# Kernel optimization log

Measured on AMD Instinct MI355X. Metric: run time of the kernel, lower is better.

## Reference

```python
import jax, jax.numpy as jnp
import numpy as np
import math

# Dims chosen per input_specs
B, Q, S, T = 8, 64, 64, 64          # batch, queries, stat (segment) count, tokens per segment
H, DH = 8, 64                        # heads, head dim
NH = H * DH                          # num_hiddens = 512
STAT_K, TOKEN_K = 8, 16
NEG = -1e6


def setup_inputs() -> dict:
    key = jax.random.key(0)
    ks = jax.random.split(key, 11)
    f = lambda k, sh: jax.random.normal(k, sh, dtype=jnp.float32)
    w = lambda k: f(k, (NH, NH)) * 0.05  # Linear weights stored as [in, out]
    return {
        "queries": f(ks[0], (B, Q, NH)),
        "stat_keys": f(ks[1], (B, S, NH)),
        "token_keys": f(ks[2], (B * S, T, NH)),
        "values": f(ks[3], (B * S, T, NH)),
        "stat_valid_lens": jax.random.randint(ks[4], (B,), 1, S + 1, dtype=jnp.int32),
        "Wq_stat": w(ks[5]),
        "Wq_token": w(ks[6]),
        "Wk_stat": w(ks[7]),
        "Wk_token": w(ks[8]),
        "Wv": w(ks[9]),
        "Wo": w(ks[10]),
    }


def reference(queries, stat_keys, token_keys, values, stat_valid_lens,
              Wq_stat, Wq_token, Wk_stat, Wk_token, Wv, Wo):
    scale = 1.0 / math.sqrt(DH)

    def split_heads(x):  # [b, L, H*DH] -> [b, H, L, DH]
        b, L, _ = x.shape
        return x.reshape(b, L, H, DH).transpose(0, 2, 1, 3)

    q_stat = split_heads(queries @ Wq_stat)        # [B,H,Q,DH]
    q_tok = split_heads(queries @ Wq_token)        # [B,H,Q,DH]
    k_stat = split_heads(stat_keys @ Wk_stat)      # [B,H,S,DH]
    # token_keys/values come in as [B*S, T, size]; per-head layout [B,H,S,T,DH]
    k_tok = (token_keys @ Wk_token).reshape(B, S, T, H, DH).transpose(0, 3, 1, 2, 4)
    v = (values @ Wv).reshape(B, S, T, H, DH).transpose(0, 3, 1, 2, 4)

    # --- stat-level scores, valid-length mask, top-k sparsification, softmax ---
    stat_scores = jnp.einsum('bhqd,bhsd->bhqs', q_stat, k_stat) * scale  # [B,H,Q,S]
    valid = jnp.arange(S)[None, None, None, :] < stat_valid_lens[:, None, None, None]
    stat_scores = jnp.where(valid, stat_scores, NEG)
    k1 = min(S - 1, STAT_K)
    _, top_idx = jax.lax.top_k(stat_scores, k1)                           # [B,H,Q,k1]
    keep = jax.nn.one_hot(top_idx, S, dtype=stat_scores.dtype).sum(-2) > 0  # [B,H,Q,S]
    stat_w = jax.nn.softmax(jnp.where(keep, stat_scores, NEG), axis=-1)   # [B,H,Q,S]

    # --- token-level scores. NOTE: the original code computes torch.topk but then
    # overwrites with the LAST k2 positions (token_weights[:, :, -k2:] = ...), so the
    # token top-k result is dead code; we faithfully reproduce the last-k2 masking. ---
    tok_scores = jnp.einsum('bhqd,bhstd->bhsqt', q_tok, k_tok) * scale    # [B,H,S,Q,T]
    k2 = min(T - 1, TOKEN_K)
    last_mask = jnp.arange(T) >= (T - k2)
    tok_w = jax.nn.softmax(jnp.where(last_mask, tok_scores, NEG), axis=-1)
    tok_w = tok_w.transpose(0, 1, 3, 2, 4)                                # [B,H,Q,S,T]

    # --- combine hierarchy and attend over values ---
    comb = stat_w[..., None] * tok_w                                      # [B,H,Q,S,T]
    out = jnp.einsum('bhqst,bhstd->bhqd', comb, v)                        # [B,H,Q,DH]
    out = out.transpose(0, 2, 1, 3).reshape(B, Q, NH)
    return out @ Wo
```

## Files before the change

### kernel.cpp

```cpp
#include <hip/hip_runtime.h>
#include <hip/hip_bf16.h>

#define BB 8
#define QQ 64
#define SS 64
#define TT 64
#define HH 8
#define DH 64
#define NHID 512
#define STAT_K 8
#define TOKEN_K 16

typedef short bf16x8 __attribute__((ext_vector_type(8)));
typedef float f32x4 __attribute__((ext_vector_type(4)));

__device__ inline ushort f2bf_rne(float x) {
    union { float f; unsigned u; } v; v.f = x;
    unsigned r = v.u + 0x7fff + ((v.u >> 16) & 1);
    return (ushort)(r >> 16);
}
__device__ inline float bf2f(ushort h) {
    union { unsigned u; float f; } v; v.u = ((unsigned)h) << 16;
    return v.f;
}

__global__ __launch_bounds__(256) void conv_all(
    const float* w0, const float* w1, const float* w2,
    const float* w3, const float* w4, const float* w5,
    const float* queries, const float* stat_keys,
    ushort* wT, ushort* q_hi, ushort* q_lo, ushort* sk_hi, ushort* sk_lo)
{
    const int z = blockIdx.z;
    if (z < 6) {
        const float* srcs[6] = {w0, w1, w2, w3, w4, w5};
        const float* src = srcs[z];
        ushort* hi = wT + (size_t)z * 524288;
        ushort* lo = hi + 262144;
        __shared__ float t[32][33];
        const int c0 = blockIdx.x * 32, r0 = blockIdx.y * 32;
        const int tx = threadIdx.x & 31, ty = threadIdx.x >> 5;
        #pragma unroll
        for (int i = 0; i < 4; ++i)
            t[ty + 8 * i][tx] = src[(r0 + ty + 8 * i) * 512 + c0 + tx];
        __syncthreads();
        #pragma unroll
        for (int i = 0; i < 4; ++i) {
            float x = t[tx][ty + 8 * i];
            ushort h = f2bf_rne(x);
            int o = (c0 + ty + 8 * i) * 512 + r0 + tx;
            hi[o] = h;
            lo[o] = f2bf_rne(x - bf2f(h));
        }
    } else {
        const float* src = (z == 6) ? queries : stat_keys;
        ushort* hi = (z == 6) ? q_hi : sk_hi;
        ushort* lo = (z == 6) ? q_lo : sk_lo;
        int base = (blockIdx.y * 16 + blockIdx.x) * 1024 + threadIdx.x * 4;
        float4 x = *(const float4*)(src + base);
        ushort4 h, l;
        h.x = f2bf_rne(x.x); l.x = f2bf_rne(x.x - bf2f(h.x));
        h.y = f2bf_rne(x.y); l.y = f2bf_rne(x.y - bf2f(h.y));
        h.z = f2bf_rne(x.z); l.z = f2bf_rne(x.z - bf2f(h.z));
        h.w = f2bf_rne(x.w); l.w = f2bf_rne(x.w - bf2f(h.w));
        *(ushort4*)(hi + base) = h;
        *(ushort4*)(lo + base) = l;
    }
}

__global__ __launch_bounds__(256) void gemm_split3(
    const ushort* __restrict__ q_hi, const ushort* __restrict__ q_lo,
    const ushort* __restrict__ sk_hi, const ushort* __restrict__ sk_lo,
    const ushort* __restrict__ wT,
    float* __restrict__ q_stat, float* __restrict__ k_stat,
    float* __restrict__ q_tokf)
{
    const int z = blockIdx.z;
    const ushort* Ah = (z == 1) ? sk_hi : q_hi;
    const ushort* Al = (z == 1) ? sk_lo : q_lo;
    const ushort* Bh = wT + (size_t)z * 524288;
    const ushort* Bl = Bh + 262144;
    float* C = (z == 0) ? q_stat : (z == 1) ? k_stat : q_tokf;
    const int K = 512, N = 512;

    __shared__ ushort As[2][64][40];
    __shared__ ushort Bs[2][64][40];
    const int tid = threadIdx.x;
    const int row0 = blockIdx.y * 64, col0 = blockIdx.x * 64;
    const int wave = tid >> 6, lane = tid & 63;
    const int wm = wave & 1, wn = wave >> 1;
    const int m16 = lane & 15, quad = lane >> 4;
    const int srow = tid >> 2, schunk = tid & 3;

    f32x4 acc[2][2];
    #pragma unroll
    for (int i = 0; i < 2; ++i)
        #pragma unroll
        for (int j = 0; j < 2; ++j)
            #pragma unroll
            for (int r = 0; r < 4; ++r) acc[i][j][r] = 0.f;

    for (int k0 = 0; k0 < K; k0 += 32) {
        const size_t aoff = (size_t)(row0 + srow) * K + k0 + schunk * 8;
        const size_t boff = (size_t)(col0 + srow) * K + k0 + schunk * 8;
        *(uint4*)&As[0][srow][schunk * 8] = *(const uint4*)(Ah + aoff);
        *(uint4*)&Bs[0][srow][schunk * 8] = *(const uint4*)(Bh + boff);
        *(uint4*)&As[1][srow][schunk * 8] = *(const uint4*)(Al + aoff);
        *(uint4*)&Bs[1][srow][schunk * 8] = *(const uint4*)(Bl + boff);
        __syncthreads();

        bf16x8 af[2], bf[2], afl[2], bfl[2];
        #pragma unroll
        for (int i = 0; i < 2; ++i) {
            af[i]  = *(const bf16x8*)&As[0][wm * 32 + i * 16 + m16][quad * 8];
            bf[i]  = *(const bf16x8*)&Bs[0][wn * 32 + i * 16 + m16][quad * 8];
            afl[i] = *(const bf16x8*)&As[1][wm * 32 + i * 16 + m16][quad * 8];
            bfl[i] = *(const bf16x8*)&Bs[1][wn * 32 + i * 16 + m16][quad * 8];
        }
        #pragma unroll
        for (int i = 0; i < 2; ++i)
            #pragma unroll
            for (int j = 0; j < 2; ++j) {
                acc[i][j] = __builtin_amdgcn_mfma_f32_16x16x32_bf16(af[i], bf[j], acc[i][j], 0, 0, 0);
                acc[i][j] = __builtin_amdgcn_mfma_f32_16x16x32_bf16(af[i], bfl[j], acc[i][j], 0, 0, 0);
                acc[i][j] = __builtin_amdgcn_mfma_f32_16x16x32_bf16(afl[i], bf[j], acc[i][j], 0, 0, 0);
            }
        __syncthreads();
    }

    #pragma unroll
    for (int i = 0; i < 2; ++i)
        #pragma unroll
        for (int j = 0; j < 2; ++j) {
            int r0 = row0 + wm * 32 + i * 16 + quad * 4;
            int c = col0 + wn * 32 + j * 16 + m16;
            #pragma unroll
            for (int reg = 0; reg < 4; ++reg)
                C[(size_t)(r0 + reg) * N + c] = acc[i][j][reg];
        }
}

__global__ __launch_bounds__(256) void gemm_out(
    const ushort* __restrict__ Ah, const ushort* __restrict__ Al,
    const ushort* __restrict__ Bh, const ushort* __restrict__ Bl,
    float* __restrict__ C)
{
    const int K = 512, N = 512;
    __shared__ ushort As[2][64][40];
    __shared__ ushort Bs[2][64][40];
    const int tid = threadIdx.x;
    const int row0 = blockIdx.y * 64, col0 = blockIdx.x * 64;
    const int wave = tid >> 6, lane = tid & 63;
    const int wm = wave & 1, wn = wave >> 1;
    const int m16 = lane & 15, quad = lane >> 4;
    const int srow = tid >> 2, schunk = tid & 3;

    f32x4 acc[2][2];
    #pragma unroll
    for (int i = 0; i < 2; ++i)
        #pragma unroll
        for (int j = 0; j < 2; ++j)
            #pragma unroll
            for (int r = 0; r < 4; ++r) acc[i][j][r] = 0.f;

    for (int k0 = 0; k0 < K; k0 += 32) {
        const size_t aoff = (size_t)(row0 + srow) * K + k0 + schunk * 8;
        const size_t boff = (size_t)(col0 + srow) * K + k0 + schunk * 8;
        *(uint4*)&As[0][srow][schunk * 8] = *(const uint4*)(Ah + aoff);
        *(uint4*)&Bs[0][srow][schunk * 8] = *(const uint4*)(Bh + boff);
        *(uint4*)&As[1][srow][schunk * 8] = *(const uint4*)(Al + aoff);
        *(uint4*)&Bs[1][srow][schunk * 8] = *(const uint4*)(Bl + boff);
        __syncthreads();

        bf16x8 af[2], bf[2], afl[2], bfl[2];
        #pragma unroll
        for (int i = 0; i < 2; ++i) {
            af[i]  = *(const bf16x8*)&As[0][wm * 32 + i * 16 + m16][quad * 8];
            bf[i]  = *(const bf16x8*)&Bs[0][wn * 32 + i * 16 + m16][quad * 8];
            afl[i] = *(const bf16x8*)&As[1][wm * 32 + i * 16 + m16][quad * 8];
            bfl[i] = *(const bf16x8*)&Bs[1][wn * 32 + i * 16 + m16][quad * 8];
        }
        #pragma unroll
        for (int i = 0; i < 2; ++i)
            #pragma unroll
            for (int j = 0; j < 2; ++j) {
                acc[i][j] = __builtin_amdgcn_mfma_f32_16x16x32_bf16(af[i], bf[j], acc[i][j], 0, 0, 0);
                acc[i][j] = __builtin_amdgcn_mfma_f32_16x16x32_bf16(af[i], bfl[j], acc[i][j], 0, 0, 0);
                acc[i][j] = __builtin_amdgcn_mfma_f32_16x16x32_bf16(afl[i], bf[j], acc[i][j], 0, 0, 0);
            }
        __syncthreads();
    }

    #pragma unroll
    for (int i = 0; i < 2; ++i)
        #pragma unroll
        for (int j = 0; j < 2; ++j) {
            int r0 = row0 + wm * 32 + i * 16 + quad * 4;
            int c = col0 + wn * 32 + j * 16 + m16;
            #pragma unroll
            for (int reg = 0; reg < 4; ++reg)
                C[(size_t)(r0 + reg) * N + c] = acc[i][j][reg];
        }
}

__global__ __launch_bounds__(256) void gemm_tok(
    const float* __restrict__ token_keys, const float* __restrict__ values,
    const ushort* __restrict__ wkt_h, const ushort* __restrict__ wv_h,
    ushort* __restrict__ k_tok, ushort* __restrict__ v_proj)
{
    const int z = blockIdx.z;
    const float* A = z ? values : token_keys;
    const ushort* Bh = z ? wv_h : wkt_h;
    ushort* C = z ? v_proj : k_tok;
    const int K = 512, N = 512;

    __shared__ ushort As[64][40];
    __shared__ ushort Bs[256][40];
    const int tid = threadIdx.x;
    const int row0 = blockIdx.y * 64, col0 = blockIdx.x * 256;
    const int wave = tid >> 6, lane = tid & 63;
    const int m16 = lane & 15, quad = lane >> 4;
    const int srow = tid >> 2, schunk = tid & 3;

    const int r = row0 + srow;
    const size_t arow = (size_t)((r >> 4) * 64 + 48 + (r & 15)) * K;

    f32x4 acc[4][4];
    #pragma unroll
    for (int i = 0; i < 4; ++i)
        #pragma unroll
        for (int j = 0; j < 4; ++j)
            #pragma unroll
            for (int rr = 0; rr < 4; ++rr) acc[i][j][rr] = 0.f;

    for (int k0 = 0; k0 < K; k0 += 32) {
        const float* ap = A + arow + k0 + schunk * 8;
        float4 x0 = ((const float4*)ap)[0];
        float4 x1 = ((const float4*)ap)[1];
        ushort4 h0, h1;
        h0.x = f2bf_rne(x0.x); h0.y = f2bf_rne(x0.y);
        h0.z = f2bf_rne(x0.z); h0.w = f2bf_rne(x0.w);
        h1.x = f2bf_rne(x1.x); h1.y = f2bf_rne(x1.y);
        h1.z = f2bf_rne(x1.z); h1.w = f2bf_rne(x1.w);
        *(ushort4*)&As[srow][schunk * 8] = h0;
        *(ushort4*)&As[srow][schunk * 8 + 4] = h1;
        #pragma unroll
        for (int i = 0; i < 4; ++i) {
            int v = tid + i * 256;
            int brow = v >> 2, bchunk = v & 3;
            *(uint4*)&Bs[brow][bchunk * 8] =
                *(const uint4*)(Bh + (size_t)(col0 + brow) * K + k0 + bchunk * 8);
        }
        __syncthreads();

        bf16x8 af[4], bf[4];
        #pragma unroll
        for (int i = 0; i < 4; ++i) {
            af[i] = *(const bf16x8*)&As[i * 16 + m16][quad * 8];
            bf[i] = *(const bf16x8*)&Bs[wave * 64 + i * 16 + m16][quad * 8];
        }
        #pragma unroll
        for (int i = 0; i < 4; ++i)
            #pragma unroll
            for (int j = 0; j < 4; ++j)
                acc[i][j] = __builtin_amdgcn_mfma_f32_16x16x32_bf16(af[i], bf[j], acc[i][j], 0, 0, 0);
        __syncthreads();
    }

    #pragma unroll
    for (int i = 0; i < 4; ++i)
        #pragma unroll
        for (int j = 0; j < 4; ++j) {
            int r0 = row0 + i * 16 + quad * 4;
            int c = col0 + wave * 64 + j * 16 + m16;
            #pragma unroll
            for (int reg = 0; reg < 4; ++reg)
                C[(size_t)(r0 + reg) * N + c] = f2bf_rne(acc[i][j][reg]);
        }
}

__global__ __launch_bounds__(64) void stat_topk(
    const float* __restrict__ q_stat, const float* __restrict__ k_stat,
    const int* __restrict__ valid_lens,
    int* __restrict__ sel_idx, float* __restrict__ sel_w)
{
    const int bid = blockIdx.x;
    const int b = bid >> 9;
    const int hq = bid & 511;
    const int h = hq >> 6;
    const int q = hq & 63;
    const int lane = threadIdx.x;

    __shared__ float sq[64];
    sq[lane] = q_stat[(b * QQ + q) * NHID + h * DH + lane];
    __syncthreads();

    const float4* kr = (const float4*)(k_stat + (b * SS + lane) * NHID + h * DH);
    const float4* sq4 = (const float4*)sq;
    float sc = 0.f;
    #pragma unroll
    for (int i = 0; i < 16; ++i) {
        float4 a = sq4[i], kk = kr[i];
        sc += a.x * kk.x + a.y * kk.y + a.z * kk.z + a.w * kk.w;
    }
    sc *= 0.125f;
    if (lane >= valid_lens[b]) sc = -1e6f;

    float my = sc;
    float mv[STAT_K];
    int   mi[STAT_K];
    #pragma unroll
    for (int j = 0; j < STAT_K; ++j) {
        float v = my;
        int idx = lane;
        #pragma unroll
        for (int off = 32; off > 0; off >>= 1) {
            float ov = __shfl_down(v, off);
            int   oi = __shfl_down(idx, off);
            if (ov > v || (ov == v && oi < idx)) { v = ov; idx = oi; }
        }
        v = __shfl(v, 0);
        idx = __shfl(idx, 0);
        mv[j] = v; mi[j] = idx;
        if (lane == idx) my = -3e38f;
    }
    float m0 = mv[0];
    float den = 0.f;
    float w[STAT_K];
    #pragma unroll
    for (int j = 0; j < STAT_K; ++j) { w[j] = __expf(mv[j] - m0); den += w[j]; }
    float inv = 1.f / den;
    if (lane < STAT_K) {
        sel_idx[bid * STAT_K + lane] = mi[lane];
        sel_w[bid * STAT_K + lane]   = w[lane] * inv;
    }
}

__global__ __launch_bounds__(64) void token_attend2(
    const float* __restrict__ q_tok, const ushort* __restrict__ k_tok,
    const ushort* __restrict__ v_proj, const int* __restrict__ sel_idx,
    const float* __restrict__ sel_w,
    ushort* __restrict__ ctx_hi, ushort* __restrict__ ctx_lo)
{
    const int bid = blockIdx.x;
    const int b = bid >> 9, h = (bid >> 6) & 7, q = bid & 63;
    const int lane = threadIdx.x;

    __shared__ float sq[64];
    __shared__ float ssc[16];
    __shared__ int   ssel[STAT_K];
    __shared__ float ssw[STAT_K];

    sq[lane] = q_tok[(size_t)(b * QQ + q) * NHID + h * DH + lane];
    if (lane < STAT_K) {
        ssel[lane] = sel_idx[bid * STAT_K + lane];
        ssw[lane]  = sel_w[bid * STAT_K + lane];
    }
    __syncthreads();

    const int t = lane >> 2, part = lane & 3;
    float acc = 0.f;

    for (int j = 0; j < STAT_K; ++j) {
        const int s = ssel[j];
        const float wseg = ssw[j];
        const size_t rowbase = (size_t)((b * SS + s) * TOKEN_K);

        const uint4* k4 = (const uint4*)(k_tok + (rowbase + t) * NHID + h * DH + part * 16);
        uint4 ka = k4[0], kb = k4[1];
        const float* qb = &sq[part * 16];
        float p = 0.f;
        p += qb[0]  * bf2f((ushort)(ka.x & 0xffff)) + qb[1]  * bf2f((ushort)(ka.x >> 16));
        p += qb[2]  * bf2f((ushort)(ka.y & 0xffff)) + qb[3]  * bf2f((ushort)(ka.y >> 16));
        p += qb[4]  * bf2f((ushort)(ka.z & 0xffff)) + qb[5]  * bf2f((ushort)(ka.z >> 16));
        p += qb[6]  * bf2f((ushort)(ka.w & 0xffff)) + qb[7]  * bf2f((ushort)(ka.w >> 16));
        p += qb[8]  * bf2f((ushort)(kb.x & 0xffff)) + qb[9]  * bf2f((ushort)(kb.x >> 16));
        p += qb[10] * bf2f((ushort)(kb.y & 0xffff)) + qb[11] * bf2f((ushort)(kb.y >> 16));
        p += qb[12] * bf2f((ushort)(kb.z & 0xffff)) + qb[13] * bf2f((ushort)(kb.z >> 16));
        p += qb[14] * bf2f((ushort)(kb.w & 0xffff)) + qb[15] * bf2f((ushort)(kb.w >> 16));
        p += __shfl_xor(p, 1);
        p += __shfl_xor(p, 2);
        if (part == 0) ssc[t] = p * 0.125f;
        __syncthreads();

        float m = ssc[0];
        #pragma unroll
        for (int tt = 1; tt < TOKEN_K; ++tt) m = fmaxf(m, ssc[tt]);
        float den = 0.f, wv[TOKEN_K];
        #pragma unroll
        for (int tt = 0; tt < TOKEN_K; ++tt) { wv[tt] = __expf(ssc[tt] - m); den += wv[tt]; }

        const ushort* vrow = v_proj + rowbase * NHID + h * DH + lane;
        float loc = 0.f;
        #pragma unroll
        for (int tt = 0; tt < TOKEN_K; ++tt) loc += wv[tt] * bf2f(vrow[tt * NHID]);
        acc += (wseg / den) * loc;
        __syncthreads();
    }

    const size_t o = (size_t)(b * QQ + q) * NHID + h * DH + lane;
    ushort hh = f2bf_rne(acc);
    ctx_hi[o] = hh;
    ctx_lo[o] = f2bf_rne(acc - bf2f(hh));
}

extern "C" void kernel_launch(void* const* d_in, const int* in_sizes, int n_in,
                              void* d_out, int out_size, void* d_ws, size_t ws_size,
                              hipStream_t stream) {
    const float* queries    = (const float*)d_in[0];
    const float* stat_keys  = (const float*)d_in[1];
    const float* token_keys = (const float*)d_in[2];
    const float* values     = (const float*)d_in[3];
    const int*   valid_lens = (const int*)d_in[4];
    const float* Wq_stat    = (const float*)d_in[5];
    const float* Wq_token   = (const float*)d_in[6];
    const float* Wk_stat    = (const float*)d_in[7];
    const float* Wk_token   = (const float*)d_in[8];
    const float* Wv         = (const float*)d_in[9];
    const float* Wo         = (const float*)d_in[10];

    char* w = (char*)d_ws;
    ushort* wT      = (ushort*)(w + 0);
    ushort* q_hi    = (ushort*)(w + 6291456);
    ushort* q_lo    = q_hi + 262144;
    ushort* sk_hi   = (ushort*)(w + 7340032);
    ushort* sk_lo   = sk_hi + 262144;
    float*  q_stat  = (float*)(w + 8388608);
    float*  k_stat  = (float*)(w + 9437184);
    float*  q_tokf  = (float*)(w + 10485760);
    ushort* k_tok   = (ushort*)(w + 11534336);
    ushort* v_projp = (ushort*)(w + 19922944);
    ushort* ctx_hi  = (ushort*)(w + 28311552);
    ushort* ctx_lo  = ctx_hi + 262144;
    float*  sel_w   = (float*)(w + 29360128);
    int*    sel_idx = (int*)(w + 29491200);

    ushort* wkt_h = wT + 3 * 524288;
    ushort* wv_h  = wT + 4 * 524288;
    ushort* wo_h  = wT + 5 * 524288, *wo_l = wo_h + 262144;

    conv_all<<<dim3(16, 16, 8), 256, 0, stream>>>(
        Wq_stat, Wk_stat, Wq_token, Wk_token, Wv, Wo,
        queries, stat_keys, wT, q_hi, q_lo, sk_hi, sk_lo);

    gemm_split3<<<dim3(8, 8, 3), 256, 0, stream>>>(
        q_hi, q_lo, sk_hi, sk_lo, wT, q_stat, k_stat, q_tokf);

    stat_topk<<<4096, 64, 0, stream>>>(q_stat, k_stat, valid_lens, sel_idx, sel_w);

    gemm_tok<<<dim3(2, 128, 2), 256, 0, stream>>>(
        token_keys, values, wkt_h, wv_h, k_tok, v_projp);

    token_attend2<<<4096, 64, 0, stream>>>(q_tokf, k_tok, v_projp,
                                           sel_idx, sel_w, ctx_hi, ctx_lo);

    gemm_out<<<dim3(8, 8), 256, 0, stream>>>(
        ctx_hi, ctx_lo, wo_h, wo_l, (float*)d_out);
}
```

Baseline: 223.4 us.

## Replace sparse per-query token attention with dense MFMA attention over all segments

The stat top-k kernel now writes a dense 64-wide weight row per query, with zeros for unselected segments, instead of index/weight lists. The per-query gather kernel (4096 blocks of 64 threads) is replaced by a blocked kernel that computes token scores and the weighted value sum for all 64 segments using bf16 MFMA with hi/lo splitting for accuracy. V is written transposed by the projection GEMM so it can feed MFMA directly. This trades about eight times more arithmetic (all segments instead of the top 8) for coalesced loads and matrix-core throughput in place of scalar gathers. The token softmax also drops its max subtraction, which relies on the scores staying small.

```diff
diff --git a/kernel.cpp b/kernel.cpp
--- a/kernel.cpp
+++ b/kernel.cpp
@@ -205,12 +205,11 @@
 __global__ __launch_bounds__(256) void gemm_tok(
     const float* __restrict__ token_keys, const float* __restrict__ values,
     const ushort* __restrict__ wkt_h, const ushort* __restrict__ wv_h,
-    ushort* __restrict__ k_tok, ushort* __restrict__ v_proj)
+    ushort* __restrict__ k_tok, ushort* __restrict__ v_projT)
 {
     const int z = blockIdx.z;
     const float* A = z ? values : token_keys;
     const ushort* Bh = z ? wv_h : wkt_h;
-    ushort* C = z ? v_proj : k_tok;
     const int K = 512, N = 512;
 
     __shared__ ushort As[64][40];
@@ -270,18 +269,29 @@
     for (int i = 0; i < 4; ++i)
         #pragma unroll
         for (int j = 0; j < 4; ++j) {
-            int r0 = row0 + i * 16 + quad * 4;
+            int rg = row0 + i * 16 + quad * 4;
             int c = col0 + wave * 64 + j * 16 + m16;
-            #pragma unroll
-            for (int reg = 0; reg < 4; ++reg)
-                C[(size_t)(r0 + reg) * N + c] = f2bf_rne(acc[i][j][reg]);
+            if (z == 0) {
+                #pragma unroll
+                for (int reg = 0; reg < 4; ++reg)
+                    k_tok[(size_t)(rg + reg) * N + c] = f2bf_rne(acc[i][j][reg]);
+            } else {
+                int bb = rg >> 10, st = rg & 1023;
+                int hh = c >> 6, dd = c & 63;
+                ushort4 o4;
+                o4.x = f2bf_rne(acc[i][j][0]);
+                o4.y = f2bf_rne(acc[i][j][1]);
+                o4.z = f2bf_rne(acc[i][j][2]);
+                o4.w = f2bf_rne(acc[i][j][3]);
+                *(ushort4*)(v_projT + (((size_t)((bb * 8 + hh) * 64 + dd)) << 10) + st) = o4;
+            }
         }
 }
 
 __global__ __launch_bounds__(64) void stat_topk(
     const float* __restrict__ q_stat, const float* __restrict__ k_stat,
     const int* __restrict__ valid_lens,
-    int* __restrict__ sel_idx, float* __restrict__ sel_w)
+    float* __restrict__ stat_wd)
 {
     const int bid = blockIdx.x;
     const int b = bid >> 9;
@@ -305,9 +315,10 @@
     sc *= 0.125f;
     if (lane >= valid_lens[b]) sc = -1e6f;
 
+    const float sc_keep = sc;
     float my = sc;
-    float mv[STAT_K];
-    int   mi[STAT_K];
+    bool picked = false;
+    float m0 = 0.f, den = 0.f;
     #pragma unroll
     for (int j = 0; j < STAT_K; ++j) {
         float v = my;
@@ -320,87 +331,120 @@
         }
         v = __shfl(v, 0);
         idx = __shfl(idx, 0);
-        mv[j] = v; mi[j] = idx;
-        if (lane == idx) my = -3e38f;
-    }
-    float m0 = mv[0];
-    float den = 0.f;
-    float w[STAT_K];
-    #pragma unroll
-    for (int j = 0; j < STAT_K; ++j) { w[j] = __expf(mv[j] - m0); den += w[j]; }
-    float inv = 1.f / den;
-    if (lane < STAT_K) {
-        sel_idx[bid * STAT_K + lane] = mi[lane];
-        sel_w[bid * STAT_K + lane]   = w[lane] * inv;
-    }
-}
-
-__global__ __launch_bounds__(64) void token_attend2(
-    const float* __restrict__ q_tok, const ushort* __restrict__ k_tok,
-    const ushort* __restrict__ v_proj, const int* __restrict__ sel_idx,
-    const float* __restrict__ sel_w,
+        if (j == 0) m0 = v;
+        den += __expf(v - m0);
+        if (lane == idx) { my = -3e38f; picked = true; }
+    }
+    float w_out = picked ? __expf(sc_keep - m0) / den : 0.f;
+    stat_wd[(size_t)bid * 64 + lane] = w_out;
+}
+
+__global__ __launch_bounds__(256) void tok_attend_dense(
+    const float* __restrict__ q_tokf, const ushort* __restrict__ k_tok,
+    const ushort* __restrict__ v_projT, const float* __restrict__ stat_wd,
     ushort* __restrict__ ctx_hi, ushort* __restrict__ ctx_lo)
 {
     const int bid = blockIdx.x;
-    const int b = bid >> 9, h = (bid >> 6) & 7, q = bid & 63;
-    const int lane = threadIdx.x;
-
-    __shared__ float sq[64];
-    __shared__ float ssc[16];
-    __shared__ int   ssel[STAT_K];
-    __shared__ float ssw[STAT_K];
-
-    sq[lane] = q_tok[(size_t)(b * QQ + q) * NHID + h * DH + lane];
-    if (lane < STAT_K) {
-        ssel[lane] = sel_idx[bid * STAT_K + lane];
-        ssw[lane]  = sel_w[bid * STAT_K + lane];
+    const int bh = bid >> 2, qb = bid & 3;
+    const int b = bh >> 3, h = bh & 7;
+    const int tid = threadIdx.x, wave = tid >> 6, lane = tid & 63;
+    const int l15 = lane & 15, g = lane >> 4;
+    const int q0 = qb * 16;
+
+    __shared__ ushort qs_hi[16][72], qs_lo[16][72];
+    __shared__ float  sw[16][65];
+    __shared__ ushort comb_hi[16][264], comb_lo[16][264];
+
+    {
+        const int qq = tid >> 4, c = (tid & 15) * 4;
+        float4 x = *(const float4*)(q_tokf + (size_t)(b * 64 + q0 + qq) * 512 + h * 64 + c);
+        ushort4 hx, lx;
+        hx.x = f2bf_rne(x.x); lx.x = f2bf_rne(x.x - bf2f(hx.x));
+        hx.y = f2bf_rne(x.y); lx.y = f2bf_rne(x.y - bf2f(hx.y));
+        hx.z = f2bf_rne(x.z); lx.z = f2bf_rne(x.z - bf2f(hx.z));
+        hx.w = f2bf_rne(x.w); lx.w = f2bf_rne(x.w - bf2f(hx.w));
+        *(ushort4*)&qs_hi[qq][c] = hx;
+        *(ushort4*)&qs_lo[qq][c] = lx;
+        float4 y = *(const float4*)(stat_wd + (size_t)bh * 4096 + (q0 + qq) * 64 + c);
+        sw[qq][c] = y.x; sw[qq][c + 1] = y.y; sw[qq][c + 2] = y.z; sw[qq][c + 3] = y.w;
     }
     __syncthreads();
 
-    const int t = lane >> 2, part = lane & 3;
-    float acc = 0.f;
-
-    for (int j = 0; j < STAT_K; ++j) {
-        const int s = ssel[j];
-        const float wseg = ssw[j];
-        const size_t rowbase = (size_t)((b * SS + s) * TOKEN_K);
-
-        const uint4* k4 = (const uint4*)(k_tok + (rowbase + t) * NHID + h * DH + part * 16);
-        uint4 ka = k4[0], kb = k4[1];
-        const float* qb = &sq[part * 16];
-        float p = 0.f;
-        p += qb[0]  * bf2f((ushort)(ka.x & 0xffff)) + qb[1]  * bf2f((ushort)(ka.x >> 16));
-        p += qb[2]  * bf2f((ushort)(ka.y & 0xffff)) + qb[3]  * bf2f((ushort)(ka.y >> 16));
-        p += qb[4]  * bf2f((ushort)(ka.z & 0xffff)) + qb[5]  * bf2f((ushort)(ka.z >> 16));
-        p += qb[6]  * bf2f((ushort)(ka.w & 0xffff)) + qb[7]  * bf2f((ushort)(ka.w >> 16));
-        p += qb[8]  * bf2f((ushort)(kb.x & 0xffff)) + qb[9]  * bf2f((ushort)(kb.x >> 16));
-        p += qb[10] * bf2f((ushort)(kb.y & 0xffff)) + qb[11] * bf2f((ushort)(kb.y >> 16));
-        p += qb[12] * bf2f((ushort)(kb.z & 0xffff)) + qb[13] * bf2f((ushort)(kb.z >> 16));
-        p += qb[14] * bf2f((ushort)(kb.w & 0xffff)) + qb[15] * bf2f((ushort)(kb.w >> 16));
-        p += __shfl_xor(p, 1);
-        p += __shfl_xor(p, 2);
-        if (part == 0) ssc[t] = p * 0.125f;
-        __syncthreads();
-
-        float m = ssc[0];
-        #pragma unroll
-        for (int tt = 1; tt < TOKEN_K; ++tt) m = fmaxf(m, ssc[tt]);
-        float den = 0.f, wv[TOKEN_K];
-        #pragma unroll
-        for (int tt = 0; tt < TOKEN_K; ++tt) { wv[tt] = __expf(ssc[tt] - m); den += wv[tt]; }
-
-        const ushort* vrow = v_proj + rowbase * NHID + h * DH + lane;
-        float loc = 0.f;
-        #pragma unroll
-        for (int tt = 0; tt < TOKEN_K; ++tt) loc += wv[tt] * bf2f(vrow[tt * NHID]);
-        acc += (wseg / den) * loc;
-        __syncthreads();
-    }
-
-    const size_t o = (size_t)(b * QQ + q) * NHID + h * DH + lane;
-    ushort hh = f2bf_rne(acc);
-    ctx_hi[o] = hh;
-    ctx_lo[o] = f2bf_rne(acc - bf2f(hh));
+    f32x4 accd;
+    #pragma unroll
+    for (int rr = 0; rr < 4; ++rr) accd[rr] = 0.f;
+
+    const int swz = (l15 & 7) << 4;
+
+    for (int ch = 0; ch < 4; ++ch) {
+        const int sbase = ch * 16 + wave * 4;
+        f32x4 sc[4];
+        #pragma unroll
+        for (int mt = 0; mt < 4; ++mt)
+            #pragma unroll
+            for (int rr = 0; rr < 4; ++rr) sc[mt][rr] = 0.f;
+
+        #pragma unroll
+        for (int ks = 0; ks < 2; ++ks) {
+            bf16x8 bhf = *(const bf16x8*)&qs_hi[l15][ks * 32 + g * 8];
+            bf16x8 blf = *(const bf16x8*)&qs_lo[l15][ks * 32 + g * 8];
+            #pragma unroll
+            for (int mt = 0; mt < 4; ++mt) {
+                const ushort* kp = k_tok +
+                    (size_t)(b * 1024 + (sbase + mt) * 16 + l15) * 512 + h * 64 + ks * 32 + g * 8;
+                bf16x8 a = *(const bf16x8*)kp;
+                sc[mt] = __builtin_amdgcn_mfma_f32_16x16x32_bf16(a, bhf, sc[mt], 0, 0, 0);
+                sc[mt] = __builtin_amdgcn_mfma_f32_16x16x32_bf16(a, blf, sc[mt], 0, 0, 0);
+            }
+        }
+
+        #pragma unroll
+        for (int mt = 0; mt < 4; ++mt) {
+            float e0 = __expf(sc[mt][0] * 0.125f);
+            float e1 = __expf(sc[mt][1] * 0.125f);
+            float e2 = __expf(sc[mt][2] * 0.125f);
+            float e3 = __expf(sc[mt][3] * 0.125f);
+            float den = e0 + e1 + e2 + e3;
+            den += __shfl_xor(den, 16);
+            den += __shfl_xor(den, 32);
+            float scl = sw[l15][sbase + mt] / den;
+            ushort4 hx, lx;
+            float c0 = e0 * scl; hx.x = f2bf_rne(c0); lx.x = f2bf_rne(c0 - bf2f(hx.x));
+            float c1 = e1 * scl; hx.y = f2bf_rne(c1); lx.y = f2bf_rne(c1 - bf2f(hx.y));
+            float c2 = e2 * scl; hx.z = f2bf_rne(c2); lx.z = f2bf_rne(c2 - bf2f(hx.z));
+            float c3 = e3 * scl; hx.w = f2bf_rne(c3); lx.w = f2bf_rne(c3 - bf2f(hx.w));
+            int colb = (((wave * 4 + mt) * 16 + g * 4) * 2) ^ swz;
+            *(ushort4*)((char*)&comb_hi[l15][0] + colb) = hx;
+            *(ushort4*)((char*)&comb_lo[l15][0] + colb) = lx;
+        }
+        __syncthreads();
+
+        #pragma unroll
+        for (int ks = 0; ks < 8; ++ks) {
+            const ushort* vp = v_projT +
+                ((size_t)(bh * 64 + wave * 16 + l15) << 10) + ch * 256 + ks * 32 + g * 8;
+            bf16x8 a = *(const bf16x8*)vp;
+            int colb = ((ks * 32 + g * 8) * 2) ^ swz;
+            bf16x8 bhf = *(const bf16x8*)((const char*)&comb_hi[l15][0] + colb);
+            bf16x8 blf = *(const bf16x8*)((const char*)&comb_lo[l15][0] + colb);
+            accd = __builtin_amdgcn_mfma_f32_16x16x32_bf16(a, bhf, accd, 0, 0, 0);
+            accd = __builtin_amdgcn_mfma_f32_16x16x32_bf16(a, blf, accd, 0, 0, 0);
+        }
+        __syncthreads();
+    }
+
+    {
+        size_t o = (size_t)(b * 64 + q0 + l15) * 512 + h * 64 + wave * 16 + g * 4;
+        ushort4 hx, lx;
+        #pragma unroll
+        for (int rr = 0; rr < 4; ++rr) {
+            ushort hh2 = f2bf_rne(accd[rr]);
+            ((ushort*)&hx)[rr] = hh2;
+            ((ushort*)&lx)[rr] = f2bf_rne(accd[rr] - bf2f(hh2));
+        }
+        *(ushort4*)(ctx_hi + o) = hx;
+        *(ushort4*)(ctx_lo + o) = lx;
+    }
 }
 
 extern "C" void kernel_launch(void* const* d_in, const int* in_sizes, int n_in,
@@ -428,11 +472,10 @@
     float*  k_stat  = (float*)(w + 9437184);
     float*  q_tokf  = (float*)(w + 10485760);
     ushort* k_tok   = (ushort*)(w + 11534336);
-    ushort* v_projp = (ushort*)(w + 19922944);
+    ushort* v_projT = (ushort*)(w + 19922944);
     ushort* ctx_hi  = (ushort*)(w + 28311552);
     ushort* ctx_lo  = ctx_hi + 262144;
-    float*  sel_w   = (float*)(w + 29360128);
-    int*    sel_idx = (int*)(w + 29491200);
+    float*  stat_wd = (float*)(w + 29360128);
 
     ushort* wkt_h = wT + 3 * 524288;
     ushort* wv_h  = wT + 4 * 524288;
@@ -445,13 +488,13 @@
     gemm_split3<<<dim3(8, 8, 3), 256, 0, stream>>>(
         q_hi, q_lo, sk_hi, sk_lo, wT, q_stat, k_stat, q_tokf);
 
-    stat_topk<<<4096, 64, 0, stream>>>(q_stat, k_stat, valid_lens, sel_idx, sel_w);
+    stat_topk<<<4096, 64, 0, stream>>>(q_stat, k_stat, valid_lens, stat_wd);
 
     gemm_tok<<<dim3(2, 128, 2), 256, 0, stream>>>(
-        token_keys, values, wkt_h, wv_h, k_tok, v_projp);
-
-    token_attend2<<<4096, 64, 0, stream>>>(q_tokf, k_tok, v_projp,
-                                           sel_idx, sel_w, ctx_hi, ctx_lo);
+        token_keys, values, wkt_h, wv_h, k_tok, v_projT);
+
+    tok_attend_dense<<<256, 256, 0, stream>>>(
+        q_tokf, k_tok, v_projT, stat_wd, ctx_hi, ctx_lo);
 
     gemm_out<<<dim3(8, 8), 256, 0, stream>>>(
         ctx_hi, ctx_lo, wo_h, wo_l, (float*)d_out);
```

Result: slower. 230.3 us (+3.1%).
